# Optimization experiments

Measured on AMD Instinct MI355X. Metric: run time of the kernel, lower is better.

The kernel has to match this reference:

```python
import jax, jax.numpy as jnp
import numpy as np

N = 200      # nodes (fixed by Linear(200,100) on x.T)
E = 8000     # edges
NFEAT, NHID, NCLASS = 8192, 2048, 512


def _cheb_conv(x, edge_index, edge_weight, W, b):
    """PyG ChebConv (K=3, sym norm, lambda_max=2): L_hat = -D^{-1/2} A D^{-1/2}.
    T0 = x, T1 = L_hat x, T2 = 2 L_hat T1 - T0; out = sum_k T_k @ W[k] + b."""
    row, col = edge_index[0], edge_index[1]
    deg = jax.ops.segment_sum(edge_weight, row, num_segments=N)
    safe = jnp.where(deg > 0, deg, 1.0)
    dinv = jnp.where(deg > 0, 1.0 / jnp.sqrt(safe), 0.0)
    norm = -dinv[row] * edge_weight * dinv[col]  # [E]

    def lap(z):  # messages from source j=row to target i=col
        return jax.ops.segment_sum(norm[:, None] * z[row], col, num_segments=N)

    T1 = lap(x)
    T2 = 2.0 * lap(T1) - x
    return x @ W[0] + T1 @ W[1] + T2 @ W[2] + b


def _forward_single(x, ei, ew, W1, b1, W2, b2):
    h = jax.nn.relu(_cheb_conv(x, ei, ew, W1, b1))
    # dropout is identity in eval mode
    return _cheb_conv(h, ei, ew, W2, b2)  # [N, NCLASS]


def _classifier(z, Wc1, bc1, Wc2, bc2, Wc3, bc3):
    h = jax.nn.relu(z @ Wc1.T + bc1)
    h = jax.nn.relu(h @ Wc2.T + bc2)
    return h @ Wc3.T + bc3  # [NCLASS, 1]


def setup_inputs() -> dict:
    key = jax.random.key(0)
    ks = jax.random.split(key, 12)
    inp = {
        'x1': jax.random.normal(ks[0], (N, NFEAT), jnp.float32),
        'edge_index1': jax.random.randint(ks[1], (2, E), 0, N, jnp.int64),
        'edge_attr1': jax.random.uniform(ks[2], (E,), jnp.float32),
        'x2': jax.random.normal(ks[3], (N, NFEAT), jnp.float32),
        'edge_index2': jax.random.randint(ks[4], (2, E), 0, N, jnp.int64),
        'edge_attr2': jax.random.uniform(ks[5], (E,), jnp.float32),
        'W1': jax.random.normal(ks[6], (3, NFEAT, NHID), jnp.float32) * (NFEAT ** -0.5),
        'b1': jnp.zeros((NHID,), jnp.float32),
        'W2': jax.random.normal(ks[7], (3, NHID, NCLASS), jnp.float32) * (NHID ** -0.5),
        'b2': jnp.zeros((NCLASS,), jnp.float32),
        'Wc1': jax.random.normal(ks[8], (100, 200), jnp.float32) * (200 ** -0.5),
        'bc1': jnp.zeros((100,), jnp.float32),
        'Wc2': jax.random.normal(ks[9], (50, 100), jnp.float32) * (100 ** -0.5),
        'bc2': jnp.zeros((50,), jnp.float32),
        'Wc3': jax.random.normal(ks[10], (1, 50), jnp.float32) * (50 ** -0.5),
        'bc3': jnp.zeros((1,), jnp.float32),
    }
    return inp


def reference(x1, edge_index1, edge_attr1, x2, edge_index2, edge_attr2,
              W1, b1, W2, b2, Wc1, bc1, Wc2, bc2, Wc3, bc3):
    o1 = _forward_single(x1, edge_index1, edge_attr1, W1, b1, W2, b2)
    o2 = _forward_single(x2, edge_index2, edge_attr2, W1, b1, W2, b2)
    out1 = _classifier(o1.T, Wc1, bc1, Wc2, bc2, Wc3, bc3)  # [NCLASS, 1]
    out2 = _classifier(o2.T, Wc1, bc1, Wc2, bc2, Wc3, bc3)
    return out1, out2
```

## Files before the change

### kernel.cpp

```cpp
#include <hip/hip_runtime.h>

typedef __attribute__((ext_vector_type(8))) short short8;
typedef __attribute__((ext_vector_type(4))) float f32x4;
typedef __attribute__((ext_vector_type(2))) float f32x2;
typedef __attribute__((ext_vector_type(4))) unsigned int u32x4;

#define NNODES 200
#define NEDGE  8000
#define NF1    8192
#define NH     2048
#define NCL    512
#define K1     24576
#define K2     6144
#define MR     448
#define MV     400
#define PV     400
#define KC1    16
#define BK1    1536
#define KC2    16
#define BK2    384

#define OFF_P1  0ull
#define SZ_P1   ((unsigned long long)KC1*PV*NH*4)
#define OFF_P2  (OFF_P1 + SZ_P1)
#define SZ_P2   ((unsigned long long)KC2*PV*NCL*4)
#define OFF_A1  (OFF_P2 + SZ_P2)
#define SZ_A1   ((unsigned long long)MR*K1*2)
#define OFF_A2  (OFF_A1 + SZ_A1)
#define SZ_A2   ((unsigned long long)MR*K2*2)
#define OFF_DEG (OFF_A2 + SZ_A2)
#define OFF_LD  (OFF_DEG + 2048)
#define OFF_LL  (OFF_LD + 320000ull)
#define OFF_Z   OFF_P1

static __device__ __forceinline__ unsigned short f2bf(float f) {
  unsigned int u = __float_as_uint(f);
  unsigned int r = (u + 0x7fffu + ((u >> 16) & 1u)) >> 16;
  return (unsigned short)r;
}
static __device__ __forceinline__ unsigned packbf(float a, float b) {
  return (unsigned)f2bf(a) | ((unsigned)f2bf(b) << 16);
}

__global__ void k_zero(f32x4* p1, int n1, f32x4* p2, int n2, f32x4* p3, int n3) {
  int i = blockIdx.x * 256 + threadIdx.x;
  f32x4 z = {0.f, 0.f, 0.f, 0.f};
  if (i < n1) p1[i] = z;
  i -= n1;
  if (i >= 0 && i < n2) p2[i] = z;
  i -= n2;
  if (i >= 0 && i < n3) p3[i] = z;
}

__global__ void k_deg(const int* __restrict__ ei1, const float* __restrict__ ew1,
                      const int* __restrict__ ei2, const float* __restrict__ ew2,
                      float* __restrict__ deg) {
  int e = blockIdx.x * 256 + threadIdx.x;
  if (e >= 2 * NEDGE) return;
  int g = e / NEDGE, k = e % NEDGE;
  const int* ei = g ? ei2 : ei1;
  const float* ew = g ? ew2 : ew1;
  atomicAdd(deg + g * NNODES + ei[k], ew[k]);
}

__global__ void k_buildL(const int* __restrict__ ei1, const float* __restrict__ ew1,
                         const int* __restrict__ ei2, const float* __restrict__ ew2,
                         const float* __restrict__ deg, float* __restrict__ Ld) {
  int e = blockIdx.x * 256 + threadIdx.x;
  if (e >= 2 * NEDGE) return;
  int g = e / NEDGE, k = e % NEDGE;
  const int* ei = g ? ei2 : ei1;
  const float* ew = g ? ew2 : ew1;
  int r = ei[k], c = ei[NEDGE + k];
  float dr = deg[g * NNODES + r], dc = deg[g * NNODES + c];
  float ir = dr > 0.f ? 1.0f / sqrtf(dr) : 0.f;
  float ic = dc > 0.f ? 1.0f / sqrtf(dc) : 0.f;
  float nrm = -ir * ew[k] * ic;
  atomicAdd(Ld + ((size_t)g * NNODES + c) * NNODES + r, nrm);
}

__global__ void k_LL(const float* __restrict__ Ld, unsigned short* __restrict__ LLb) {
  int b = blockIdx.x;
  int g = b / NNODES, i = b % NNODES;
  __shared__ float Lr[NNODES];
  const float* Lg = Ld + (size_t)g * NNODES * NNODES;
  int t = threadIdx.x;
  if (t < NNODES) Lr[t] = Lg[i * NNODES + t];
  __syncthreads();
  if (t < NNODES) {
    float acc = 0.f;
    for (int k = 0; k < NNODES; ++k) acc = fmaf(Lr[k], Lg[k * NNODES + t], acc);
    unsigned short* LLg = LLb + (size_t)g * MR * 224;
    LLg[(size_t)i * 224 + t] = f2bf(Lr[t]);
    LLg[(size_t)(NNODES + i) * 224 + t] = f2bf(2.f * acc - (i == t ? 1.f : 0.f));
  }
}

__global__ void k_t0(const float* __restrict__ x1, const float* __restrict__ x2,
                     unsigned short* __restrict__ A1) {
  int gid = blockIdx.x * 256 + threadIdx.x;
  int row = gid / (NF1 / 8);
  int c8 = (gid % (NF1 / 8)) * 8;
  const float* xp = (row < NNODES ? x1 + (size_t)row * NF1
                                  : x2 + (size_t)(row - NNODES) * NF1) + c8;
  f32x4 a = *(const f32x4*)xp;
  f32x4 b = *(const f32x4*)(xp + 4);
  u32x4 o;
  o[0] = packbf(a[0], a[1]);
  o[1] = packbf(a[2], a[3]);
  o[2] = packbf(b[0], b[1]);
  o[3] = packbf(b[2], b[3]);
  *(u32x4*)(A1 + (size_t)row * K1 + c8) = o;
}

__global__ __launch_bounds__(256, 1)
void k_abuild(const unsigned short* __restrict__ LLb, const unsigned short* __restrict__ Asrc,
              unsigned short* __restrict__ Adst, const int Nf, const int Ka) {
  __shared__ __align__(16) unsigned short XF[7][4][64][8];
  const int g = blockIdx.x & 1;
  const int nt = blockIdx.x >> 1;
  const int nbase = nt * 64;
  const int t = threadIdx.x;

  #pragma unroll
  for (int it = 0; it < 14; ++it) {
    const int pos = it * 256 + t;
    const int j = pos >> 4;
    const int n4 = (pos & 15) * 4;
    unsigned long long v = 0ull;
    if (j < NNODES)
      v = *(const unsigned long long*)(Asrc + (size_t)(g * NNODES + j) * Ka + nbase + n4);
    const int ks = j >> 5, kg = (j >> 3) & 3, jj = j & 7;
    #pragma unroll
    for (int e = 0; e < 4; ++e) {
      const int nn = n4 + e;
      XF[ks][nn >> 4][(nn & 15) + 16 * kg][jj] = (unsigned short)(v >> (16 * e));
    }
  }
  __syncthreads();

  const int w = t >> 6, lane = t & 63;
  const int lm = lane & 15, lk8 = (lane >> 4) * 8;
  f32x4 acc[7][4];
  #pragma unroll
  for (int i = 0; i < 7; ++i)
    #pragma unroll
    for (int j = 0; j < 4; ++j) acc[i][j] = (f32x4){0.f, 0.f, 0.f, 0.f};

  const unsigned short* LLg = LLb + (size_t)g * MR * 224;
  #pragma unroll
  for (int ks = 0; ks < 7; ++ks) {
    short8 bfr[4];
    #pragma unroll
    for (int nf = 0; nf < 4; ++nf) bfr[nf] = *(const short8*)&XF[ks][nf][lane][0];
    short8 af[7];
    #pragma unroll
    for (int mf = 0; mf < 7; ++mf)
      af[mf] = *(const short8*)(LLg + (size_t)(w * 112 + mf * 16 + lm) * 224 + ks * 32 + lk8);
    #pragma unroll
    for (int mf = 0; mf < 7; ++mf)
      #pragma unroll
      for (int nf = 0; nf < 4; ++nf)
        acc[mf][nf] = __builtin_amdgcn_mfma_f32_16x16x32_bf16(af[mf], bfr[nf], acc[mf][nf], 0, 0, 0);
  }

  const int lr4 = (lane >> 4) * 4;
  #pragma unroll
  for (int mf = 0; mf < 7; ++mf) {
    #pragma unroll
    for (int ri = 0; ri < 4; ++ri) {
      const int m = w * 112 + mf * 16 + lr4 + ri;
      if (m < MV) {
        const int drow = g * NNODES + (m < NNODES ? m : m - NNODES);
        const size_t dbase = (size_t)drow * Ka + (m < NNODES ? Nf : 2 * Nf) + nbase + lm;
        #pragma unroll
        for (int nf = 0; nf < 4; ++nf)
          Adst[dbase + nf * 16] = f2bf(acc[mf][nf][ri]);
      }
    }
  }
}

template <int BN, int KA, int KC>
__global__ __launch_bounds__(512, 2)
void k_gemm(const float* __restrict__ W, const unsigned short* __restrict__ A,
            float* __restrict__ P, const int Nn, const int BK) {
  constexpr int NF = BN / 16;
  constexpr int NFW = BN / 32;
  constexpr int CW = BN / 16;
  constexpr int ABUF = MR * 128;
  constexpr int BSTRIDE = NF * 1024;
  constexpr int WBUF = 2 * BSTRIDE;
  __shared__ __align__(16) unsigned short Atile[2 * MR * 64];
  __shared__ __align__(16) unsigned short Wt[2 * NF * 1024];

  const int t = threadIdx.x;
  const int w = t >> 6, lane = t & 63;
  const int wm = w >> 1, wn = w & 1;
  const int lm = lane & 15;
  const int l4 = lane >> 4;
  const int kc = blockIdx.x % KC;
  const int nt = blockIdx.x / KC;
  const int kbase = kc * BK;
  const int nbase = nt * BN;
  const int nks = BK >> 6;

  const int arow0 = t >> 3;
  const int agb = ((t * 16) & 127) ^ ((arow0 & 7) << 4);
  const char* Ab = (const char*)A + (size_t)kbase * 2 + (size_t)arow0 * (KA * 2) + agb;
  const size_t CSTEP = (size_t)64 * KA * 2;

  const int kk0 = (t >> 4) * 2;
  const int colb = (t & 15) * CW;
  const float* Wg = W + (size_t)(kbase + kk0) * Nn + nbase + colb;
  int offWl[CW];
  {
    const int ks0 = kk0 >> 5, kg0 = (kk0 >> 3) & 3, jj1 = (kk0 & 7) >> 1;
    #pragma unroll
    for (int e = 0; e < CW; ++e) {
      const int nn = colb + e;
      const int nf = nn >> 4;
      const int ln = ((nn & 15) + 16 * kg0) ^ (nf & 3);
      offWl[e] = ((ks0 * NF + nf) * 64 + ln) * 4 + jj1;
    }
  }

  const int aBase = (wm * 112 + lm) * 128 + ((l4 * 16) ^ ((lm & 7) << 4));
  int bAddr[NFW];
  #pragma unroll
  for (int nf = 0; nf < NFW; ++nf) {
    const int nfg = wn * NFW + nf;
    bAddr[nf] = nfg * 1024 + (lane ^ (nfg & 3)) * 16;
  }

  f32x4 acc[7][NFW];
  #pragma unroll
  for (int i = 0; i < 7; ++i)
    #pragma unroll
    for (int j = 0; j < NFW; ++j) acc[i][j] = (f32x4){0.f, 0.f, 0.f, 0.f};

  u32x4 areg[7];
  f32x4 w0a, w0b, w1a, w1b;
  f32x2 w0s, w1s;

  auto loadW = [&](int kt) {
    const float* p = Wg + (size_t)kt * 64 * Nn;
    if constexpr (BN == 128) {
      w0a = __builtin_nontemporal_load((const f32x4*)p);
      w0b = __builtin_nontemporal_load((const f32x4*)(p + 4));
      w1a = __builtin_nontemporal_load((const f32x4*)(p + Nn));
      w1b = __builtin_nontemporal_load((const f32x4*)(p + Nn + 4));
    } else if constexpr (BN == 64) {
      w0a = __builtin_nontemporal_load((const f32x4*)p);
      w1a = __builtin_nontemporal_load((const f32x4*)(p + Nn));
    } else {
      w0s = __builtin_nontemporal_load((const f32x2*)p);
      w1s = __builtin_nontemporal_load((const f32x2*)(p + Nn));
    }
  };
  auto loadA = [&](int kt) {
    #pragma unroll
    for (int c = 0; c < 7; ++c)
      areg[c] = *(const u32x4*)(Ab + c * CSTEP + (size_t)kt * 128);
  };
  auto storeA = [&](int buf) {
    #pragma unroll
    for (int c = 0; c < 7; ++c)
      *(u32x4*)((char*)Atile + buf * ABUF + c * 8192 + t * 16) = areg[c];
  };
  auto storeW = [&](int buf) {
    unsigned* w32 = (unsigned*)Wt + buf * (WBUF / 4);
    #pragma unroll
    for (int e = 0; e < CW; ++e) {
      float lo, hi;
      if constexpr (BN == 128) {
        lo = (e < 4) ? w0a[e & 3] : w0b[e & 3];
        hi = (e < 4) ? w1a[e & 3] : w1b[e & 3];
      } else if constexpr (BN == 64) {
        lo = w0a[e & 3];
        hi = w1a[e & 3];
      } else {
        lo = w0s[e & 1];
        hi = w1s[e & 1];
      }
      w32[offWl[e]] = packbf(lo, hi);
    }
  };

  loadW(0);
  loadA(0);
  storeA(0);
  storeW(0);
  __syncthreads();

  for (int kt = 0; kt < nks; ++kt) {
    const int buf = kt & 1;
    const bool more = (kt + 1 < nks);
    if (more) loadW(kt + 1);

    #pragma unroll
    for (int ks = 0; ks < 2; ++ks) {
      short8 bfr[NFW];
      #pragma unroll
      for (int nf = 0; nf < NFW; ++nf)
        bfr[nf] = *(const short8*)((const char*)Wt + buf * WBUF + bAddr[nf] + ks * BSTRIDE);
      const int abx = (aBase ^ (ks * 64)) + buf * ABUF;
      short8 af[7];
      #pragma unroll
      for (int mf = 0; mf < 7; ++mf)
        af[mf] = *(const short8*)((const char*)Atile + abx + mf * 2048);
      #pragma unroll
      for (int mf = 0; mf < 7; ++mf)
        #pragma unroll
        for (int nf = 0; nf < NFW; ++nf)
          acc[mf][nf] = __builtin_amdgcn_mfma_f32_16x16x32_bf16(af[mf], bfr[nf], acc[mf][nf], 0, 0, 0);
      if (ks == 0 && more) loadA(kt + 1);
    }

    if (more) {
      storeA(buf ^ 1);
      storeW(buf ^ 1);
    }
    __syncthreads();
  }

  float* Pk = P + ((size_t)kc * PV) * Nn + nbase;
  #pragma unroll
  for (int mf = 0; mf < 7; ++mf) {
    const int row0 = wm * 112 + mf * 16 + l4 * 4;
    #pragma unroll
    for (int ri = 0; ri < 4; ++ri) {
      const int row = row0 + ri;
      if (row < MV) {
        #pragma unroll
        for (int nf = 0; nf < NFW; ++nf) {
          const int col = (wn * NFW + nf) * 16 + lm;
          __builtin_nontemporal_store(acc[mf][nf][ri], Pk + (size_t)row * Nn + col);
        }
      }
    }
  }
}

__global__ void k_ep1(const float* __restrict__ P1, const float* __restrict__ b1,
                      unsigned short* __restrict__ A2) {
  int gid = blockIdx.x * 256 + threadIdx.x;
  int row = gid / (NH / 4);
  int c = (gid % (NH / 4)) * 4;
  f32x4 s = {0.f, 0.f, 0.f, 0.f};
  #pragma unroll
  for (int kc = 0; kc < KC1; ++kc)
    s += __builtin_nontemporal_load((const f32x4*)(P1 + ((size_t)kc * PV + row) * NH + c));
  const f32x4 b = *(const f32x4*)(b1 + c);
  unsigned long long pack = 0;
  #pragma unroll
  for (int i = 0; i < 4; ++i) {
    float v = s[i] + b[i];
    pack |= (unsigned long long)f2bf(v > 0.f ? v : 0.f) << (16 * i);
  }
  *(unsigned long long*)(A2 + (size_t)row * K2 + c) = pack;
}

__global__ __launch_bounds__(256)
void k_zsum(const float* __restrict__ P2, const float* __restrict__ b2,
            float* __restrict__ zt) {
  __shared__ float tile[8][264];
  const int b = blockIdx.x;
  const int g = b / 50;
  const int r2 = b % 50;
  const int j0 = (r2 >> 1) * 8;
  const int ch = (r2 & 1) * 256;
  const int t = threadIdx.x;
  const int j = t >> 5;
  const int c0 = (t & 31) * 8;
  const int row = g * NNODES + j0 + j;

  #pragma unroll
  for (int ci = 0; ci < 2; ++ci) {
    const int c = c0 + ci * 4;
    f32x4 s = *(const f32x4*)(b2 + ch + c);
    #pragma unroll
    for (int kc = 0; kc < KC2; ++kc)
      s += __builtin_nontemporal_load((const f32x4*)(P2 + ((size_t)kc * PV + row) * NCL + ch + c));
    *(f32x4*)&tile[j][c] = s;
  }
  __syncthreads();

  f32x4 lo, hi;
  #pragma unroll
  for (int e = 0; e < 4; ++e) { lo[e] = tile[e][t]; hi[e] = tile[4 + e][t]; }
  float* zr = zt + ((size_t)g * NCL + ch + t) * 200 + j0;
  *(f32x4*)zr = lo;
  *(f32x4*)(zr + 4) = hi;
}

__global__ __launch_bounds__(256)
void k_cls2(const float* __restrict__ zt,
            const float* __restrict__ Wc1, const float* __restrict__ bc1,
            const float* __restrict__ Wc2, const float* __restrict__ bc2,
            const float* __restrict__ Wc3, const float* __restrict__ bc3,
            float* __restrict__ outp) {
  __shared__ float W1s[100 * 201];
  __shared__ float W2s[50 * 101];
  __shared__ float zs[4][200];
  __shared__ float h1s[4][104];
  __shared__ float h2s[4][56];
  const int g = blockIdx.x >> 7;
  const int t = threadIdx.x;
  const int w = t >> 6, lane = t & 63;
  const int r = (blockIdx.x & 127) * 4 + w;

  for (int i = t; i < 20000; i += 256) {
    const int c = i / 200, j = i - c * 200;
    W1s[c * 201 + j] = Wc1[i];
  }
  for (int i = t; i < 5000; i += 256) {
    const int c = i / 100, j = i - c * 100;
    W2s[c * 101 + j] = Wc2[i];
  }
  const float* zr = zt + ((size_t)g * NCL + r) * 200;
  #pragma unroll
  for (int i = 0; i < 4; ++i) {
    const int idx = i * 64 + lane;
    if (idx < 200) zs[w][idx] = zr[idx];
  }
  __syncthreads();

  {
    const int c1 = lane + 64;
    const int c1m = (c1 < 100) ? c1 : 99;
    float a0 = bc1[lane];
    float a1 = bc1[c1m];
    #pragma unroll 4
    for (int j = 0; j < 200; ++j) {
      const float zv = zs[w][j];
      a0 = fmaf(zv, W1s[lane * 201 + j], a0);
      a1 = fmaf(zv, W1s[c1m * 201 + j], a1);
    }
    h1s[w][lane] = a0 > 0.f ? a0 : 0.f;
    if (c1 < 100) h1s[w][c1] = a1 > 0.f ? a1 : 0.f;
  }
  __syncthreads();

  {
    const int c2 = (lane < 50) ? lane : 49;
    float b = bc2[c2];
    #pragma unroll 4
    for (int c = 0; c < 100; ++c) b = fmaf(h1s[w][c], W2s[c2 * 101 + c], b);
    if (lane < 50) h2s[w][lane] = b > 0.f ? b : 0.f;
  }
  __syncthreads();

  {
    float v = (lane < 50) ? h2s[w][lane] * Wc3[lane] : 0.f;
    #pragma unroll
    for (int off = 32; off >= 1; off >>= 1) v += __shfl_down(v, off);
    if (lane == 0) outp[g * NCL + r] = v + bc3[0];
  }
}

extern "C" void kernel_launch(void* const* d_in, const int* in_sizes, int n_in,
                              void* d_out, int out_size, void* d_ws, size_t ws_size,
                              hipStream_t stream) {
  const float* x1  = (const float*)d_in[0];
  const int*   ei1 = (const int*)d_in[1];
  const float* ea1 = (const float*)d_in[2];
  const float* x2  = (const float*)d_in[3];
  const int*   ei2 = (const int*)d_in[4];
  const float* ea2 = (const float*)d_in[5];
  const float* W1  = (const float*)d_in[6];
  const float* b1  = (const float*)d_in[7];
  const float* W2  = (const float*)d_in[8];
  const float* b2  = (const float*)d_in[9];
  const float* Wc1 = (const float*)d_in[10];
  const float* bc1 = (const float*)d_in[11];
  const float* Wc2 = (const float*)d_in[12];
  const float* bc2 = (const float*)d_in[13];
  const float* Wc3 = (const float*)d_in[14];
  const float* bc3 = (const float*)d_in[15];
  float* outp = (float*)d_out;

  char* ws = (char*)d_ws;
  float*          P1  = (float*)(ws + OFF_P1);
  float*          P2  = (float*)(ws + OFF_P2);
  unsigned short* A1  = (unsigned short*)(ws + OFF_A1);
  unsigned short* A2  = (unsigned short*)(ws + OFF_A2);
  float*          deg = (float*)(ws + OFF_DEG);
  float*          Ld  = (float*)(ws + OFF_LD);
  unsigned short* LLb = (unsigned short*)(ws + OFF_LL);
  float*          zt  = (float*)(ws + OFF_Z);

  k_zero<<<897, 256, 0, stream>>>(
      (f32x4*)(ws + OFF_DEG), 45216,
      (f32x4*)(ws + OFF_A1 + (size_t)MV * K1 * 2), 147456,
      (f32x4*)(ws + OFF_A2 + (size_t)MV * K2 * 2), 36864);

  k_deg<<<63, 256, 0, stream>>>(ei1, ea1, ei2, ea2, deg);
  k_buildL<<<63, 256, 0, stream>>>(ei1, ea1, ei2, ea2, deg, Ld);
  k_LL<<<400, 256, 0, stream>>>(Ld, LLb);
  k_t0<<<1600, 256, 0, stream>>>(x1, x2, A1);
  k_abuild<<<(NF1 / 64) * 2, 256, 0, stream>>>(LLb, A1, A1, NF1, K1);
  k_gemm<128, K1, KC1><<<KC1 * (NH / 128), 512, 0, stream>>>(W1, A1, P1, NH, BK1);
  k_ep1<<<800, 256, 0, stream>>>(P1, b1, A2);
  k_abuild<<<(NH / 64) * 2, 256, 0, stream>>>(LLb, A2, A2, NH, K2);
  k_gemm<32, K2, KC2><<<KC2 * (NCL / 32), 512, 0, stream>>>(W2, A2, P2, NCL, BK2);
  k_zsum<<<100, 256, 0, stream>>>(P2, b2, zt);
  k_cls2<<<256, 256, 0, stream>>>(zt, Wc1, bc1, Wc2, bc2, Wc3, bc3, outp);
}
```

Measured before the change: 177.6 us.

## Fuse degree and Laplacian build into one kernel; prefetch weights two tiles ahead

The separate degree and Laplacian-build kernels are merged into a single two-block kernel that accumulates degrees in shared memory, which removes one launch and the global deg buffer. The GEMM main loop now keeps two register sets for weights so W is loaded two k-tiles ahead, and the A prefetch moves to between the two k-substeps. The loop is unrolled by two to alternate the register sets, which assumes an even tile count, and the extra weight registers raise register pressure. The graph kernel runs on only two blocks, so edge processing is less parallel.

```diff
diff --git a/kernel.cpp b/kernel.cpp
--- a/kernel.cpp
+++ b/kernel.cpp
@@ -28,8 +28,7 @@
 #define SZ_A1   ((unsigned long long)MR*K1*2)
 #define OFF_A2  (OFF_A1 + SZ_A1)
 #define SZ_A2   ((unsigned long long)MR*K2*2)
-#define OFF_DEG (OFF_A2 + SZ_A2)
-#define OFF_LD  (OFF_DEG + 2048)
+#define OFF_LD  (OFF_A2 + SZ_A2)
 #define OFF_LL  (OFF_LD + 320000ull)
 #define OFF_Z   OFF_P1
 
@@ -52,31 +51,31 @@
   if (i >= 0 && i < n3) p3[i] = z;
 }
 
-__global__ void k_deg(const int* __restrict__ ei1, const float* __restrict__ ew1,
-                      const int* __restrict__ ei2, const float* __restrict__ ew2,
-                      float* __restrict__ deg) {
-  int e = blockIdx.x * 256 + threadIdx.x;
-  if (e >= 2 * NEDGE) return;
-  int g = e / NEDGE, k = e % NEDGE;
+__global__ __launch_bounds__(1024)
+void k_graph(const int* __restrict__ ei1, const float* __restrict__ ew1,
+             const int* __restrict__ ei2, const float* __restrict__ ew2,
+             float* __restrict__ Ld) {
+  __shared__ float degs[NNODES];
+  const int g = blockIdx.x;
   const int* ei = g ? ei2 : ei1;
   const float* ew = g ? ew2 : ew1;
-  atomicAdd(deg + g * NNODES + ei[k], ew[k]);
-}
-
-__global__ void k_buildL(const int* __restrict__ ei1, const float* __restrict__ ew1,
-                         const int* __restrict__ ei2, const float* __restrict__ ew2,
-                         const float* __restrict__ deg, float* __restrict__ Ld) {
-  int e = blockIdx.x * 256 + threadIdx.x;
-  if (e >= 2 * NEDGE) return;
-  int g = e / NEDGE, k = e % NEDGE;
-  const int* ei = g ? ei2 : ei1;
-  const float* ew = g ? ew2 : ew1;
-  int r = ei[k], c = ei[NEDGE + k];
-  float dr = deg[g * NNODES + r], dc = deg[g * NNODES + c];
-  float ir = dr > 0.f ? 1.0f / sqrtf(dr) : 0.f;
-  float ic = dc > 0.f ? 1.0f / sqrtf(dc) : 0.f;
-  float nrm = -ir * ew[k] * ic;
-  atomicAdd(Ld + ((size_t)g * NNODES + c) * NNODES + r, nrm);
+  const int t = threadIdx.x;
+
+  if (t < NNODES) degs[t] = 0.f;
+  __syncthreads();
+  for (int e = t; e < NEDGE; e += 1024) atomicAdd(&degs[ei[e]], ew[e]);
+  __syncthreads();
+  if (t < NNODES) {
+    float d = degs[t];
+    degs[t] = d > 0.f ? 1.0f / sqrtf(d) : 0.f;
+  }
+  __syncthreads();
+  float* Lg = Ld + (size_t)g * NNODES * NNODES;
+  for (int e = t; e < NEDGE; e += 1024) {
+    int r = ei[e], c = ei[NEDGE + e];
+    float nrm = -degs[r] * ew[e] * degs[c];
+    atomicAdd(Lg + (size_t)c * NNODES + r, nrm);
+  }
 }
 
 __global__ void k_LL(const float* __restrict__ Ld, unsigned short* __restrict__ LLb) {
@@ -181,6 +180,12 @@
   }
 }
 
+template <int BN>
+struct WSet {
+  f32x4 a, b, c, d;
+  f32x2 s0, s1;
+};
+
 template <int BN, int KA, int KC>
 __global__ __launch_bounds__(512, 2)
 void k_gemm(const float* __restrict__ W, const unsigned short* __restrict__ A,
@@ -240,22 +245,18 @@
     for (int j = 0; j < NFW; ++j) acc[i][j] = (f32x4){0.f, 0.f, 0.f, 0.f};
 
   u32x4 areg[7];
-  f32x4 w0a, w0b, w1a, w1b;
-  f32x2 w0s, w1s;
-
-  auto loadW = [&](int kt) {
+  WSet<BN> setA, setB;
+
+  auto loadW = [&](int kt, WSet<BN>& s) {
     const float* p = Wg + (size_t)kt * 64 * Nn;
     if constexpr (BN == 128) {
-      w0a = __builtin_nontemporal_load((const f32x4*)p);
-      w0b = __builtin_nontemporal_load((const f32x4*)(p + 4));
-      w1a = __builtin_nontemporal_load((const f32x4*)(p + Nn));
-      w1b = __builtin_nontemporal_load((const f32x4*)(p + Nn + 4));
-    } else if constexpr (BN == 64) {
-      w0a = __builtin_nontemporal_load((const f32x4*)p);
-      w1a = __builtin_nontemporal_load((const f32x4*)(p + Nn));
+      s.a = __builtin_nontemporal_load((const f32x4*)p);
+      s.b = __builtin_nontemporal_load((const f32x4*)(p + 4));
+      s.c = __builtin_nontemporal_load((const f32x4*)(p + Nn));
+      s.d = __builtin_nontemporal_load((const f32x4*)(p + Nn + 4));
     } else {
-      w0s = __builtin_nontemporal_load((const f32x2*)p);
-      w1s = __builtin_nontemporal_load((const f32x2*)(p + Nn));
+      s.s0 = __builtin_nontemporal_load((const f32x2*)p);
+      s.s1 = __builtin_nontemporal_load((const f32x2*)(p + Nn));
     }
   };
   auto loadA = [&](int kt) {
@@ -268,60 +269,61 @@
     for (int c = 0; c < 7; ++c)
       *(u32x4*)((char*)Atile + buf * ABUF + c * 8192 + t * 16) = areg[c];
   };
-  auto storeW = [&](int buf) {
+  auto storeW = [&](const WSet<BN>& s, int buf) {
     unsigned* w32 = (unsigned*)Wt + buf * (WBUF / 4);
     #pragma unroll
     for (int e = 0; e < CW; ++e) {
       float lo, hi;
       if constexpr (BN == 128) {
-        lo = (e < 4) ? w0a[e & 3] : w0b[e & 3];
-        hi = (e < 4) ? w1a[e & 3] : w1b[e & 3];
-      } else if constexpr (BN == 64) {
-        lo = w0a[e & 3];
-        hi = w1a[e & 3];
+        lo = (e < 4) ? s.a[e & 3] : s.b[e & 3];
+        hi = (e < 4) ? s.c[e & 3] : s.d[e & 3];
       } else {
-        lo = w0s[e & 1];
-        hi = w1s[e & 1];
+        lo = s.s0[e & 1];
+        hi = s.s1[e & 1];
       }
       w32[offWl[e]] = packbf(lo, hi);
     }
   };
-
-  loadW(0);
-  loadA(0);
-  storeA(0);
-  storeW(0);
-  __syncthreads();
-
-  for (int kt = 0; kt < nks; ++kt) {
-    const int buf = kt & 1;
-    const bool more = (kt + 1 < nks);
-    if (more) loadW(kt + 1);
-
-    #pragma unroll
-    for (int ks = 0; ks < 2; ++ks) {
-      short8 bfr[NFW];
+  auto compute = [&](int buf, int ks) {
+    short8 bfr[NFW];
+    #pragma unroll
+    for (int nf = 0; nf < NFW; ++nf)
+      bfr[nf] = *(const short8*)((const char*)Wt + buf * WBUF + bAddr[nf] + ks * BSTRIDE);
+    const int abx = (aBase ^ (ks * 64)) + buf * ABUF;
+    short8 af[7];
+    #pragma unroll
+    for (int mf = 0; mf < 7; ++mf)
+      af[mf] = *(const short8*)((const char*)Atile + abx + mf * 2048);
+    #pragma unroll
+    for (int mf = 0; mf < 7; ++mf)
       #pragma unroll
       for (int nf = 0; nf < NFW; ++nf)
-        bfr[nf] = *(const short8*)((const char*)Wt + buf * WBUF + bAddr[nf] + ks * BSTRIDE);
-      const int abx = (aBase ^ (ks * 64)) + buf * ABUF;
-      short8 af[7];
-      #pragma unroll
-      for (int mf = 0; mf < 7; ++mf)
-        af[mf] = *(const short8*)((const char*)Atile + abx + mf * 2048);
-      #pragma unroll
-      for (int mf = 0; mf < 7; ++mf)
-        #pragma unroll
-        for (int nf = 0; nf < NFW; ++nf)
-          acc[mf][nf] = __builtin_amdgcn_mfma_f32_16x16x32_bf16(af[mf], bfr[nf], acc[mf][nf], 0, 0, 0);
-      if (ks == 0 && more) loadA(kt + 1);
-    }
-
-    if (more) {
+        acc[mf][nf] = __builtin_amdgcn_mfma_f32_16x16x32_bf16(af[mf], bfr[nf], acc[mf][nf], 0, 0, 0);
+  };
+
+  loadW(0, setA);
+  loadA(0);
+  loadW(1, setB);
+  storeA(0);
+  storeW(setA, 0);
+  __syncthreads();
+
+  auto body = [&](int kt, WSet<BN>& thisSet, WSet<BN>& nextSet) {
+    const int buf = kt & 1;
+    compute(buf, 0);
+    if (kt + 1 < nks) loadA(kt + 1);
+    if (kt + 2 < nks) loadW(kt + 2, thisSet);
+    compute(buf, 1);
+    if (kt + 1 < nks) {
       storeA(buf ^ 1);
-      storeW(buf ^ 1);
+      storeW(nextSet, buf ^ 1);
     }
     __syncthreads();
+  };
+
+  for (int kt = 0; kt < nks; kt += 2) {
+    body(kt, setA, setB);
+    body(kt + 1, setB, setA);
   }
 
   float* Pk = P + ((size_t)kc * PV) * Nn + nbase;
@@ -485,18 +487,16 @@
   float*          P2  = (float*)(ws + OFF_P2);
   unsigned short* A1  = (unsigned short*)(ws + OFF_A1);
   unsigned short* A2  = (unsigned short*)(ws + OFF_A2);
-  float*          deg = (float*)(ws + OFF_DEG);
   float*          Ld  = (float*)(ws + OFF_LD);
   unsigned short* LLb = (unsigned short*)(ws + OFF_LL);
   float*          zt  = (float*)(ws + OFF_Z);
 
   k_zero<<<897, 256, 0, stream>>>(
-      (f32x4*)(ws + OFF_DEG), 45216,
+      (f32x4*)(ws + OFF_LD), 45088,
       (f32x4*)(ws + OFF_A1 + (size_t)MV * K1 * 2), 147456,
       (f32x4*)(ws + OFF_A2 + (size_t)MV * K2 * 2), 36864);
 
-  k_deg<<<63, 256, 0, stream>>>(ei1, ea1, ei2, ea2, deg);
-  k_buildL<<<63, 256, 0, stream>>>(ei1, ea1, ei2, ea2, deg, Ld);
+  k_graph<<<2, 1024, 0, stream>>>(ei1, ea1, ei2, ea2, Ld);
   k_LL<<<400, 256, 0, stream>>>(Ld, LLb);
   k_t0<<<1600, 256, 0, stream>>>(x1, x2, A1);
   k_abuild<<<(NF1 / 64) * 2, 256, 0, stream>>>(LLb, A1, A1, NF1, K1);
```

After: 228.5 us. 1.29x slower.

## Fuse graph build into one kernel and reduce GEMM2 split-K via atomics

Applied to the files above, without the earlier changes.

Degree computation and Laplacian construction are merged into one kernel per graph. It accumulates in shared memory and then writes the dense Laplacian out. The second GEMM now atomically adds its split-K partials directly into the transposed z buffer, and the bias moves into the classifier. This removes the partial buffer and the separate reduction kernel, cutting launches and memory traffic. In exchange it uses global atomics, a very large shared-memory allocation, and only two blocks for the graph build.

```diff
diff --git a/kernel.cpp b/kernel.cpp
--- a/kernel.cpp
+++ b/kernel.cpp
@@ -22,16 +22,13 @@
 
 #define OFF_P1  0ull
 #define SZ_P1   ((unsigned long long)KC1*PV*NH*4)
-#define OFF_P2  (OFF_P1 + SZ_P1)
-#define SZ_P2   ((unsigned long long)KC2*PV*NCL*4)
-#define OFF_A1  (OFF_P2 + SZ_P2)
+#define OFF_A1  (OFF_P1 + SZ_P1)
 #define SZ_A1   ((unsigned long long)MR*K1*2)
 #define OFF_A2  (OFF_A1 + SZ_A1)
 #define SZ_A2   ((unsigned long long)MR*K2*2)
-#define OFF_DEG (OFF_A2 + SZ_A2)
-#define OFF_LD  (OFF_DEG + 2048)
+#define OFF_LD  (OFF_A2 + SZ_A2)
 #define OFF_LL  (OFF_LD + 320000ull)
-#define OFF_Z   OFF_P1
+#define OFF_Z   (OFF_LL + 401408ull)
 
 static __device__ __forceinline__ unsigned short f2bf(float f) {
   unsigned int u = __float_as_uint(f);
@@ -52,31 +49,34 @@
   if (i >= 0 && i < n3) p3[i] = z;
 }
 
-__global__ void k_deg(const int* __restrict__ ei1, const float* __restrict__ ew1,
-                      const int* __restrict__ ei2, const float* __restrict__ ew2,
-                      float* __restrict__ deg) {
-  int e = blockIdx.x * 256 + threadIdx.x;
-  if (e >= 2 * NEDGE) return;
-  int g = e / NEDGE, k = e % NEDGE;
+__global__ __launch_bounds__(1024)
+void k_graph(const int* __restrict__ ei1, const float* __restrict__ ew1,
+             const int* __restrict__ ei2, const float* __restrict__ ew2,
+             float* __restrict__ Ld) {
+  __shared__ float Ls[NNODES * NNODES];
+  __shared__ float degs[NNODES];
+  const int g = blockIdx.x;
   const int* ei = g ? ei2 : ei1;
   const float* ew = g ? ew2 : ew1;
-  atomicAdd(deg + g * NNODES + ei[k], ew[k]);
-}
-
-__global__ void k_buildL(const int* __restrict__ ei1, const float* __restrict__ ew1,
-                         const int* __restrict__ ei2, const float* __restrict__ ew2,
-                         const float* __restrict__ deg, float* __restrict__ Ld) {
-  int e = blockIdx.x * 256 + threadIdx.x;
-  if (e >= 2 * NEDGE) return;
-  int g = e / NEDGE, k = e % NEDGE;
-  const int* ei = g ? ei2 : ei1;
-  const float* ew = g ? ew2 : ew1;
-  int r = ei[k], c = ei[NEDGE + k];
-  float dr = deg[g * NNODES + r], dc = deg[g * NNODES + c];
-  float ir = dr > 0.f ? 1.0f / sqrtf(dr) : 0.f;
-  float ic = dc > 0.f ? 1.0f / sqrtf(dc) : 0.f;
-  float nrm = -ir * ew[k] * ic;
-  atomicAdd(Ld + ((size_t)g * NNODES + c) * NNODES + r, nrm);
+  const int t = threadIdx.x;
+
+  for (int i = t; i < NNODES * NNODES; i += 1024) Ls[i] = 0.f;
+  if (t < NNODES) degs[t] = 0.f;
+  __syncthreads();
+  for (int e = t; e < NEDGE; e += 1024) atomicAdd(&degs[ei[e]], ew[e]);
+  __syncthreads();
+  if (t < NNODES) {
+    float d = degs[t];
+    degs[t] = d > 0.f ? 1.0f / sqrtf(d) : 0.f;
+  }
+  __syncthreads();
+  for (int e = t; e < NEDGE; e += 1024) {
+    int r = ei[e], c = ei[NEDGE + e];
+    atomicAdd(&Ls[c * NNODES + r], -degs[r] * ew[e] * degs[c]);
+  }
+  __syncthreads();
+  float* Lg = Ld + (size_t)g * NNODES * NNODES;
+  for (int i = t; i < NNODES * NNODES; i += 1024) Lg[i] = Ls[i];
 }
 
 __global__ void k_LL(const float* __restrict__ Ld, unsigned short* __restrict__ LLb) {
@@ -181,7 +181,7 @@
   }
 }
 
-template <int BN, int KA, int KC>
+template <int BN, int KA, int KC, bool AZ>
 __global__ __launch_bounds__(512, 2)
 void k_gemm(const float* __restrict__ W, const unsigned short* __restrict__ A,
             float* __restrict__ P, const int Nn, const int BK) {
@@ -250,9 +250,6 @@
       w0b = __builtin_nontemporal_load((const f32x4*)(p + 4));
       w1a = __builtin_nontemporal_load((const f32x4*)(p + Nn));
       w1b = __builtin_nontemporal_load((const f32x4*)(p + Nn + 4));
-    } else if constexpr (BN == 64) {
-      w0a = __builtin_nontemporal_load((const f32x4*)p);
-      w1a = __builtin_nontemporal_load((const f32x4*)(p + Nn));
     } else {
       w0s = __builtin_nontemporal_load((const f32x2*)p);
       w1s = __builtin_nontemporal_load((const f32x2*)(p + Nn));
@@ -276,9 +273,6 @@
       if constexpr (BN == 128) {
         lo = (e < 4) ? w0a[e & 3] : w0b[e & 3];
         hi = (e < 4) ? w1a[e & 3] : w1b[e & 3];
-      } else if constexpr (BN == 64) {
-        lo = w0a[e & 3];
-        hi = w1a[e & 3];
       } else {
         lo = w0s[e & 1];
         hi = w1s[e & 1];
@@ -324,18 +318,38 @@
     __syncthreads();
   }
 
-  float* Pk = P + ((size_t)kc * PV) * Nn + nbase;
-  #pragma unroll
-  for (int mf = 0; mf < 7; ++mf) {
-    const int row0 = wm * 112 + mf * 16 + l4 * 4;
-    #pragma unroll
-    for (int ri = 0; ri < 4; ++ri) {
-      const int row = row0 + ri;
-      if (row < MV) {
-        #pragma unroll
-        for (int nf = 0; nf < NFW; ++nf) {
-          const int col = (wn * NFW + nf) * 16 + lm;
-          __builtin_nontemporal_store(acc[mf][nf][ri], Pk + (size_t)row * Nn + col);
+  if constexpr (!AZ) {
+    float* Pk = P + ((size_t)kc * PV) * Nn + nbase;
+    #pragma unroll
+    for (int mf = 0; mf < 7; ++mf) {
+      const int row0 = wm * 112 + mf * 16 + l4 * 4;
+      #pragma unroll
+      for (int ri = 0; ri < 4; ++ri) {
+        const int row = row0 + ri;
+        if (row < MV) {
+          #pragma unroll
+          for (int nf = 0; nf < NFW; ++nf) {
+            const int col = (wn * NFW + nf) * 16 + lm;
+            __builtin_nontemporal_store(acc[mf][nf][ri], Pk + (size_t)row * Nn + col);
+          }
+        }
+      }
+    }
+  } else {
+    #pragma unroll
+    for (int mf = 0; mf < 7; ++mf) {
+      const int row0 = wm * 112 + mf * 16 + l4 * 4;
+      #pragma unroll
+      for (int ri = 0; ri < 4; ++ri) {
+        const int row = row0 + ri;
+        if (row < MV) {
+          const int g = (row >= NNODES) ? 1 : 0;
+          const int j = row - g * NNODES;
+          #pragma unroll
+          for (int nf = 0; nf < NFW; ++nf) {
+            const int c = nbase + (wn * NFW + nf) * 16 + lm;
+            atomicAdd(P + ((size_t)(g * NCL + c)) * 200 + j, acc[mf][nf][ri]);
+          }
         }
       }
     }
@@ -362,40 +376,7 @@
 }
 
 __global__ __launch_bounds__(256)
-void k_zsum(const float* __restrict__ P2, const float* __restrict__ b2,
-            float* __restrict__ zt) {
-  __shared__ float tile[8][264];
-  const int b = blockIdx.x;
-  const int g = b / 50;
-  const int r2 = b % 50;
-  const int j0 = (r2 >> 1) * 8;
-  const int ch = (r2 & 1) * 256;
-  const int t = threadIdx.x;
-  const int j = t >> 5;
-  const int c0 = (t & 31) * 8;
-  const int row = g * NNODES + j0 + j;
-
-  #pragma unroll
-  for (int ci = 0; ci < 2; ++ci) {
-    const int c = c0 + ci * 4;
-    f32x4 s = *(const f32x4*)(b2 + ch + c);
-    #pragma unroll
-    for (int kc = 0; kc < KC2; ++kc)
-      s += __builtin_nontemporal_load((const f32x4*)(P2 + ((size_t)kc * PV + row) * NCL + ch + c));
-    *(f32x4*)&tile[j][c] = s;
-  }
-  __syncthreads();
-
-  f32x4 lo, hi;
-  #pragma unroll
-  for (int e = 0; e < 4; ++e) { lo[e] = tile[e][t]; hi[e] = tile[4 + e][t]; }
-  float* zr = zt + ((size_t)g * NCL + ch + t) * 200 + j0;
-  *(f32x4*)zr = lo;
-  *(f32x4*)(zr + 4) = hi;
-}
-
-__global__ __launch_bounds__(256)
-void k_cls2(const float* __restrict__ zt,
+void k_cls2(const float* __restrict__ zt, const float* __restrict__ b2,
             const float* __restrict__ Wc1, const float* __restrict__ bc1,
             const float* __restrict__ Wc2, const float* __restrict__ bc2,
             const float* __restrict__ Wc3, const float* __restrict__ bc3,
@@ -418,11 +399,12 @@
     const int c = i / 100, j = i - c * 100;
     W2s[c * 101 + j] = Wc2[i];
   }
+  const float b2r = b2[r];
   const float* zr = zt + ((size_t)g * NCL + r) * 200;
   #pragma unroll
   for (int i = 0; i < 4; ++i) {
     const int idx = i * 64 + lane;
-    if (idx < 200) zs[w][idx] = zr[idx];
+    if (idx < 200) zs[w][idx] = zr[idx] + b2r;
   }
   __syncthreads();
 
@@ -482,28 +464,24 @@
 
   char* ws = (char*)d_ws;
   float*          P1  = (float*)(ws + OFF_P1);
-  float*          P2  = (float*)(ws + OFF_P2);
   unsigned short* A1  = (unsigned short*)(ws + OFF_A1);
   unsigned short* A2  = (unsigned short*)(ws + OFF_A2);
-  float*          deg = (float*)(ws + OFF_DEG);
   float*          Ld  = (float*)(ws + OFF_LD);
   unsigned short* LLb = (unsigned short*)(ws + OFF_LL);
   float*          zt  = (float*)(ws + OFF_Z);
 
-  k_zero<<<897, 256, 0, stream>>>(
-      (f32x4*)(ws + OFF_DEG), 45216,
+  k_zero<<<1018, 256, 0, stream>>>(
+      (f32x4*)(ws + OFF_LL), 76288,
       (f32x4*)(ws + OFF_A1 + (size_t)MV * K1 * 2), 147456,
       (f32x4*)(ws + OFF_A2 + (size_t)MV * K2 * 2), 36864);
 
-  k_deg<<<63, 256, 0, stream>>>(ei1, ea1, ei2, ea2, deg);
-  k_buildL<<<63, 256, 0, stream>>>(ei1, ea1, ei2, ea2, deg, Ld);
+  k_graph<<<2, 1024, 0, stream>>>(ei1, ea1, ei2, ea2, Ld);
   k_LL<<<400, 256, 0, stream>>>(Ld, LLb);
   k_t0<<<1600, 256, 0, stream>>>(x1, x2, A1);
   k_abuild<<<(NF1 / 64) * 2, 256, 0, stream>>>(LLb, A1, A1, NF1, K1);
-  k_gemm<128, K1, KC1><<<KC1 * (NH / 128), 512, 0, stream>>>(W1, A1, P1, NH, BK1);
+  k_gemm<128, K1, KC1, false><<<KC1 * (NH / 128), 512, 0, stream>>>(W1, A1, P1, NH, BK1);
   k_ep1<<<800, 256, 0, stream>>>(P1, b1, A2);
   k_abuild<<<(NH / 64) * 2, 256, 0, stream>>>(LLb, A2, A2, NH, K2);
-  k_gemm<32, K2, KC2><<<KC2 * (NCL / 32), 512, 0, stream>>>(W2, A2, P2, NCL, BK2);
-  k_zsum<<<100, 256, 0, stream>>>(P2, b2, zt);
-  k_cls2<<<256, 256, 0, stream>>>(zt, Wc1, bc1, Wc2, bc2, Wc3, bc3, outp);
-}
+  k_gemm<32, K2, KC2, true><<<KC2 * (NCL / 32), 512, 0, stream>>>(W2, A2, zt, NCL, BK2);
+  k_cls2<<<256, 256, 0, stream>>>(zt, b2, Wc1, bc1, Wc2, bc2, Wc3, bc3, outp);
+}
```

Measured after the change: 251.8 us. +41.8%, slower.
